# Kernel optimization log

Hardware: AMD Instinct MI355X
Metric: run time of the kernel (lower is better)

## Reference

```python
import jax, jax.numpy as jnp
import numpy as np
import math

B, L, D, H = 2, 2048, 1024, 16
DK = D // H

def setup_inputs() -> dict:
    key = jax.random.key(0)
    ks = jax.random.split(key, 12)
    s = 1.0 / math.sqrt(D)
    inp = {
        "Q": jax.random.normal(ks[0], (B, L, D), jnp.float32),
        "K": jax.random.normal(ks[1], (B, L, D), jnp.float32),
        "V": jax.random.normal(ks[2], (B, L, D), jnp.float32),
        "mask": jnp.tril(jnp.ones((L, L), jnp.bool_))[None, None],  # [1,1,L,L] causal
        "Wq_w": jax.random.normal(ks[3], (D, D), jnp.float32) * s,
        "Wq_b": jnp.zeros((D,), jnp.float32),
        "Wk_w": jax.random.normal(ks[4], (D, D), jnp.float32) * s,
        "Wk_b": jnp.zeros((D,), jnp.float32),
        "Wv_w": jax.random.normal(ks[5], (D, D), jnp.float32) * s,
        "Wv_b": jnp.zeros((D,), jnp.float32),
        "fc_w": jax.random.normal(ks[6], (D, D), jnp.float32) * s,
        "fc_b": jnp.zeros((D,), jnp.float32),
    }
    return inp

def reference(Q, K, V, mask, Wq_w, Wq_b, Wk_w, Wk_b, Wv_w, Wv_b, fc_w, fc_b):
    # torch Linear: y = x @ W.T + b
    def split_heads(x):
        return x.reshape(B, L, H, DK).transpose(0, 2, 1, 3)  # [B,H,L,DK]
    q = split_heads(Q @ Wq_w.T + Wq_b)
    k = split_heads(K @ Wk_w.T + Wk_b)
    v = split_heads(V @ Wv_w.T + Wv_b)
    scores = jnp.einsum("bhqd,bhkd->bhqk", q, k) / math.sqrt(DK)
    scores = jnp.where(mask, scores, jnp.float32(-1e9))
    attn = jax.nn.softmax(scores, axis=-1)
    out = jnp.einsum("bhqk,bhkd->bhqd", attn, v)
    out = out.transpose(0, 2, 1, 3).reshape(B, L, D)
    return out @ fc_w.T + fc_b
```

## Files before the change

kernel.cpp:

```cpp
#include <hip/hip_runtime.h>
#include <hip/hip_bf16.h>
#include <math.h>

typedef __attribute__((ext_vector_type(8))) short short8;
typedef __attribute__((ext_vector_type(4))) float float4v;

static constexpr int Bc = 2, Lc = 2048, Dc = 1024, Hc = 16;
static constexpr float C1 = 0.125f * 1.44269504088896f;
static constexpr float C2 = -8.0f * 1.44269504088896f;

__device__ __forceinline__ short f2bf(float x) {
    unsigned int b = __float_as_uint(x);
    return (short)((b + 0x7FFFu + ((b >> 16) & 1u)) >> 16);
}

__device__ __forceinline__ void gld16(const void* g, void* l) {
    __builtin_amdgcn_global_load_lds(
        (const __attribute__((address_space(1))) unsigned int*)g,
        (__attribute__((address_space(3))) unsigned int*)l, 16, 0, 0);
}

__global__ __launch_bounds__(256) void cvt_all(
    const float* q, const float* k, const float* v,
    const float* wq, const float* wk, const float* wv, const float* fw,
    short* qo, short* ko, short* vo,
    short* wqo, short* wko, short* wvo, short* fwo)
{
    const int z = blockIdx.y;
    const float* s; short* d; int n;
    switch (z) {
        case 0: s = q;  d = qo;  n = Bc*Lc*Dc; break;
        case 1: s = k;  d = ko;  n = Bc*Lc*Dc; break;
        case 2: s = v;  d = vo;  n = Bc*Lc*Dc; break;
        case 3: s = wq; d = wqo; n = Dc*Dc; break;
        case 4: s = wk; d = wko; n = Dc*Dc; break;
        case 5: s = wv; d = wvo; n = Dc*Dc; break;
        default: s = fw; d = fwo; n = Dc*Dc; break;
    }
    const int idx = (blockIdx.x * 256 + threadIdx.x) * 8;
    if (idx >= n) return;
    float4 lo = *reinterpret_cast<const float4*>(s + idx);
    float4 hi = *reinterpret_cast<const float4*>(s + idx + 4);
    short8 o = short8{f2bf(lo.x), f2bf(lo.y), f2bf(lo.z), f2bf(lo.w),
                      f2bf(hi.x), f2bf(hi.y), f2bf(hi.z), f2bf(hi.w)};
    *reinterpret_cast<short8*>(d + idx) = o;
}

struct GemmCtx {
    int lane, w, wm, wn, quad, l16, bm0, bn0, lrow, loct;
};
__device__ __forceinline__ void gemm_core(
    const short* __restrict__ A, const short* __restrict__ Bt,
    short* As, short* Bs, const GemmCtx& c, float4v acc[4][4])
{
    const int K = Dc;
    for (int k0 = 0; k0 < K; k0 += 32) {
#pragma unroll
        for (int rep = 0; rep < 2; ++rep) {
            const int rb = (c.w + 4 * rep) * 16;
            gld16(A  + (size_t)(c.bm0 + rb + c.lrow) * K + k0 + c.loct * 8, &As[rb * 32]);
            gld16(Bt + (size_t)(c.bn0 + rb + c.lrow) * K + k0 + c.loct * 8, &Bs[rb * 32]);
        }
        __syncthreads();
        short8 af[4], bf[4];
#pragma unroll
        for (int i = 0; i < 4; ++i)
            af[i] = *reinterpret_cast<const short8*>(&As[(c.wm * 64 + i * 16 + c.l16) * 32 + c.quad * 8]);
#pragma unroll
        for (int j = 0; j < 4; ++j)
            bf[j] = *reinterpret_cast<const short8*>(&Bs[(c.wn * 64 + j * 16 + c.l16) * 32 + c.quad * 8]);
#pragma unroll
        for (int i = 0; i < 4; ++i)
#pragma unroll
            for (int j = 0; j < 4; ++j)
                acc[i][j] = __builtin_amdgcn_mfma_f32_16x16x32_bf16(af[i], bf[j], acc[i][j], 0, 0, 0);
        __syncthreads();
    }
}
__device__ __forceinline__ GemmCtx make_ctx() {
    GemmCtx c;
    const int tid = threadIdx.x;
    c.lane = tid & 63; c.w = tid >> 6;
    c.wm = c.w >> 1;   c.wn = c.w & 1;
    c.quad = c.lane >> 4; c.l16 = c.lane & 15;
    c.bm0 = blockIdx.y * 128; c.bn0 = blockIdx.x * 128;
    c.lrow = c.lane >> 2; c.loct = c.lane & 3;
    return c;
}

__global__ __launch_bounds__(256, 2) void qkv_gemm(
    const short* __restrict__ Qb, const short* __restrict__ Kb, const short* __restrict__ Vb,
    const short* __restrict__ Wq, const short* __restrict__ Wk, const short* __restrict__ Wv,
    const float* __restrict__ bq, const float* __restrict__ bk, const float* __restrict__ bv,
    short* __restrict__ q_ws, short* __restrict__ k_ws, short* __restrict__ vT_ws)
{
    __shared__ short As[128 * 32];
    __shared__ short Bs[128 * 32];
    const int z = blockIdx.z;
    const short* A    = (z == 0) ? Qb : (z == 1) ? Kb : Vb;
    const short* Bt   = (z == 0) ? Wq : (z == 1) ? Wk : Wv;
    const float* bias = (z == 0) ? bq : (z == 1) ? bk : bv;

    GemmCtx c = make_ctx();
    float4v acc[4][4] = {};
    gemm_core(A, Bt, As, Bs, c, acc);

    if (z < 2) {
        short* C = (z == 0) ? q_ws : k_ws;
#pragma unroll
        for (int j = 0; j < 4; ++j) {
            const int col = c.bn0 + c.wn * 64 + j * 16 + c.l16;
            const float bv2 = bias[col];
#pragma unroll
            for (int i = 0; i < 4; ++i)
#pragma unroll
                for (int r = 0; r < 4; ++r) {
                    const int row = c.bm0 + c.wm * 64 + i * 16 + c.quad * 4 + r;
                    C[(size_t)row * Dc + col] = f2bf(acc[i][j][r] + bv2);
                }
        }
    } else {
#pragma unroll
        for (int j = 0; j < 4; ++j) {
            const int col = c.bn0 + c.wn * 64 + j * 16 + c.l16;
            const float bv2 = bias[col];
            const int hh = col >> 6, d = col & 63;
#pragma unroll
            for (int i = 0; i < 4; ++i)
#pragma unroll
                for (int r = 0; r < 4; ++r) {
                    const int row = c.bm0 + c.wm * 64 + i * 16 + c.quad * 4 + r;
                    const int b = row >> 11, l = row & 2047;
                    vT_ws[((size_t)((b * 16 + hh) * 64 + d)) * Lc + l] = f2bf(acc[i][j][r] + bv2);
                }
        }
    }
}

__global__ __launch_bounds__(256, 2) void out_gemm(
    const short* __restrict__ A, const short* __restrict__ Bt,
    const float* __restrict__ bias, float* __restrict__ C)
{
    __shared__ short As[128 * 32];
    __shared__ short Bs[128 * 32];
    GemmCtx c = make_ctx();
    float4v acc[4][4] = {};
    gemm_core(A, Bt, As, Bs, c, acc);
#pragma unroll
    for (int j = 0; j < 4; ++j) {
        const int col = c.bn0 + c.wn * 64 + j * 16 + c.l16;
        const float bv2 = bias[col];
#pragma unroll
        for (int i = 0; i < 4; ++i)
#pragma unroll
            for (int r = 0; r < 4; ++r) {
                const int row = c.bm0 + c.wm * 64 + i * 16 + c.quad * 4 + r;
                C[(size_t)row * Dc + col] = acc[i][j][r] + bv2;
            }
    }
}

__global__ __launch_bounds__(256, 2) void attn_flash3(
    const short* __restrict__ q_ws,
    const short* __restrict__ k_ws,
    const short* __restrict__ vT_ws,
    short* __restrict__ o_ws)
{
    __shared__ short Ks[64 * 64];
    __shared__ short Vs[80 * 64];
    __shared__ short Ps[4][16 * 40];

    const int tid  = threadIdx.x;
    const int lane = tid & 63;
    const int w    = tid >> 6;
    const int quad = lane >> 4;
    const int l16  = lane & 15;
    const int l7   = l16 & 7;

    const int id = blockIdx.x;
    const int p  = id & 15;
    const int bh = id >> 4;
    const int b  = bh >> 4, h = bh & 15;

    for (int i = tid; i < 16 * 64; i += 256) {
        const int row = 64 + (i >> 6);
        const int col = i & 63;
        const int oct = col >> 3;
        Vs[(row * 8 + (oct ^ (row & 7))) * 8 + (col & 7)] =
            (row == 64) ? (short)0x3F80 : (short)0;
    }

    const int srow = lane >> 3;
    const int soct = lane & 7;
    const size_t khead  = (size_t)(b * Lc) * Dc + h * 64;
    const size_t vthead = (size_t)(bh * 64) * Lc;
    const int xoct0 = quad ^ l7;
    const int xoct1 = (4 + quad) ^ l7;

#pragma unroll 1
    for (int ph = 0; ph < 2; ++ph) {
        const int qi  = ph ? (31 - p) : p;
        const int q0  = qi * 64;
        const int qw0 = q0 + w * 16;

        short8 qf[2];
        {
            const size_t base = ((size_t)(b * Lc + qw0 + l16)) * Dc + h * 64;
            qf[0] = *reinterpret_cast<const short8*>(&q_ws[base + quad * 8]);
            qf[1] = *reinterpret_cast<const short8*>(&q_ws[base + 32 + quad * 8]);
        }

        float4v o_acc[5] = {};

        for (int kb = 0; kb <= qi; ++kb) {
#pragma unroll
            for (int rep = 0; rep < 2; ++rep) {
                const int issue = w * 2 + rep;
                const int grow = issue * 8 + srow;
                const int goct = soct ^ (grow & 7);
                gld16(k_ws + khead + (size_t)(kb * 64 + grow) * Dc + goct * 8,
                      &Ks[issue * 512]);
                gld16(vT_ws + vthead + (size_t)grow * Lc + kb * 64 + goct * 8,
                      &Vs[issue * 512]);
            }
            __syncthreads();

            short8 vf[5][2];
#pragma unroll
            for (int dt = 0; dt < 5; ++dt) {
                vf[dt][0] = *reinterpret_cast<const short8*>(&Vs[(dt * 16 + l16) * 64 + xoct0 * 8]);
                vf[dt][1] = *reinterpret_cast<const short8*>(&Vs[(dt * 16 + l16) * 64 + xoct1 * 8]);
            }

#pragma unroll
            for (int pair = 0; pair < 2; ++pair) {
                if (kb * 64 + pair * 32 <= qw0 + 15) {
#pragma unroll
                    for (int tt = 0; tt < 2; ++tt) {
                        const int t = pair * 2 + tt;
                        short8 kf0 = *reinterpret_cast<const short8*>(&Ks[(t * 16 + l16) * 64 + xoct0 * 8]);
                        short8 kf1 = *reinterpret_cast<const short8*>(&Ks[(t * 16 + l16) * 64 + xoct1 * 8]);
                        float4v sv = {};
                        sv = __builtin_amdgcn_mfma_f32_16x16x32_bf16(qf[0], kf0, sv, 0, 0, 0);
                        sv = __builtin_amdgcn_mfma_f32_16x16x32_bf16(qf[1], kf1, sv, 0, 0, 0);
                        const int kcol = kb * 64 + t * 16 + l16;
#pragma unroll
                        for (int r = 0; r < 4; ++r) {
                            const int qrow = qw0 + quad * 4 + r;
                            const float pv = (kcol <= qrow) ? exp2f(fmaf(sv[r], C1, C2)) : 0.f;
                            Ps[w][(quad * 4 + r) * 40 + tt * 16 + l16] =
                                (short)(__float_as_uint(pv) >> 16);
                        }
                    }
                    asm volatile("s_waitcnt lgkmcnt(0)" ::: "memory");
                    short8 pf = *reinterpret_cast<const short8*>(&Ps[w][l16 * 40 + quad * 8]);
#pragma unroll
                    for (int dt = 0; dt < 5; ++dt)
                        o_acc[dt] = __builtin_amdgcn_mfma_f32_16x16x32_bf16(pf, vf[dt][pair], o_acc[dt], 0, 0, 0);
                }
            }
            __syncthreads();
        }

#pragma unroll
        for (int r = 0; r < 4; ++r) {
            const float lsum = __shfl(o_acc[4][r], quad << 4, 64);
            const float inv = 1.f / lsum;
            const int qrow = qw0 + quad * 4 + r;
#pragma unroll
            for (int dt = 0; dt < 4; ++dt)
                o_ws[((size_t)(b * Lc + qrow)) * Dc + h * 64 + dt * 16 + l16] =
                    f2bf(o_acc[dt][r] * inv);
        }
    }
}

extern "C" void kernel_launch(void* const* d_in, const int* in_sizes, int n_in,
                              void* d_out, int out_size, void* d_ws, size_t ws_size,
                              hipStream_t stream)
{
    const float* Q = (const float*)d_in[0];
    const float* K = (const float*)d_in[1];
    const float* V = (const float*)d_in[2];

    int w0 = -1;
    for (int i = 3; i + 8 <= n_in; ++i) {
        bool ok = true;
        for (int j = 0; j < 4 && ok; ++j)
            ok = (in_sizes[i + 2 * j] == Dc * Dc) && (in_sizes[i + 2 * j + 1] == Dc);
        if (ok) { w0 = i; break; }
    }
    if (w0 < 0) w0 = (n_in >= 12) ? 4 : 3;

    const float* Wq_w = (const float*)d_in[w0 + 0];
    const float* Wq_b = (const float*)d_in[w0 + 1];
    const float* Wk_w = (const float*)d_in[w0 + 2];
    const float* Wk_b = (const float*)d_in[w0 + 3];
    const float* Wv_w = (const float*)d_in[w0 + 4];
    const float* Wv_b = (const float*)d_in[w0 + 5];
    const float* fc_w = (const float*)d_in[w0 + 6];
    const float* fc_b = (const float*)d_in[w0 + 7];
    float* out = (float*)d_out;

    const size_t nel = (size_t)Bc * Lc * Dc;
    const size_t nw  = (size_t)Dc * Dc;
    short* p = (short*)d_ws;
    short* xq   = p;  p += nel;
    short* xk   = p;  p += nel;
    short* xv   = p;  p += nel;
    short* wqb  = p;  p += nw;
    short* wkb  = p;  p += nw;
    short* wvb  = p;  p += nw;
    short* fwb  = p;  p += nw;
    short* q_ws = p;  p += nel;
    short* k_ws = p;  p += nel;
    short* vT_ws= p;  p += nel;
    short* a_ws = xq;

    cvt_all<<<dim3(2048, 7), 256, 0, stream>>>(
        Q, K, V, Wq_w, Wk_w, Wv_w, fc_w, xq, xk, xv, wqb, wkb, wvb, fwb);

    qkv_gemm<<<dim3(8, 32, 3), 256, 0, stream>>>(
        xq, xk, xv, wqb, wkb, wvb, Wq_b, Wk_b, Wv_b, q_ws, k_ws, vT_ws);

    attn_flash3<<<dim3(512), 256, 0, stream>>>(q_ws, k_ws, vT_ws, a_ws);

    out_gemm<<<dim3(8, 32), 256, 0, stream>>>(a_ws, fwb, fc_b, out);
}
```

Before: 246.1 us.

## Double-buffer K/V tiles and keep P in registers via transposed score MFMA

```diff
diff --git a/kernel.cpp b/kernel.cpp
--- a/kernel.cpp
+++ b/kernel.cpp
@@ -3,7 +3,9 @@
 #include <math.h>
 
 typedef __attribute__((ext_vector_type(8))) short short8;
+typedef __attribute__((ext_vector_type(4))) short short4v;
 typedef __attribute__((ext_vector_type(4))) float float4v;
+typedef __attribute__((ext_vector_type(2))) unsigned int uint2v;
 
 static constexpr int Bc = 2, Lc = 2048, Dc = 1024, Hc = 16;
 static constexpr float C1 = 0.125f * 1.44269504088896f;
@@ -160,15 +162,14 @@
     }
 }
 
-__global__ __launch_bounds__(256, 2) void attn_flash3(
+__global__ __launch_bounds__(256, 2) void attn_flash4(
     const short* __restrict__ q_ws,
     const short* __restrict__ k_ws,
     const short* __restrict__ vT_ws,
     short* __restrict__ o_ws)
 {
-    __shared__ short Ks[64 * 64];
-    __shared__ short Vs[80 * 64];
-    __shared__ short Ps[4][16 * 40];
+    __shared__ short Ks[2][64 * 64];
+    __shared__ short Vs[2][64 * 64];
 
     const int tid  = threadIdx.x;
     const int lane = tid & 63;
@@ -182,14 +183,6 @@
     const int bh = id >> 4;
     const int b  = bh >> 4, h = bh & 15;
 
-    for (int i = tid; i < 16 * 64; i += 256) {
-        const int row = 64 + (i >> 6);
-        const int col = i & 63;
-        const int oct = col >> 3;
-        Vs[(row * 8 + (oct ^ (row & 7))) * 8 + (col & 7)] =
-            (row == 64) ? (short)0x3F80 : (short)0;
-    }
-
     const int srow = lane >> 3;
     const int soct = lane & 7;
     const size_t khead  = (size_t)(b * Lc) * Dc + h * 64;
@@ -197,11 +190,28 @@
     const int xoct0 = quad ^ l7;
     const int xoct1 = (4 + quad) ^ l7;
 
+    const short onev = (l16 == 0) ? (short)0x3F80 : (short)0;
+    const short4v vb4 = short4v{onev, onev, onev, onev};
+
+    auto stage = [&](int tile, int buf) {
+#pragma unroll
+        for (int rep = 0; rep < 2; ++rep) {
+            const int issue = w * 2 + rep;
+            const int grow = issue * 8 + srow;
+            const int goct = soct ^ (grow & 7);
+            gld16(k_ws + khead + (size_t)(tile * 64 + grow) * Dc + goct * 8,
+                  &Ks[buf][issue * 512]);
+            gld16(vT_ws + vthead + (size_t)grow * Lc + tile * 64 + goct * 8,
+                  &Vs[buf][issue * 512]);
+        }
+    };
+
 #pragma unroll 1
     for (int ph = 0; ph < 2; ++ph) {
         const int qi  = ph ? (31 - p) : p;
         const int q0  = qi * 64;
         const int qw0 = q0 + w * 16;
+        const int qrow = qw0 + l16;
 
         short8 qf[2];
         {
@@ -212,64 +222,68 @@
 
         float4v o_acc[5] = {};
 
+        stage(0, 0);
+
+#pragma unroll 1
         for (int kb = 0; kb <= qi; ++kb) {
-#pragma unroll
-            for (int rep = 0; rep < 2; ++rep) {
-                const int issue = w * 2 + rep;
-                const int grow = issue * 8 + srow;
-                const int goct = soct ^ (grow & 7);
-                gld16(k_ws + khead + (size_t)(kb * 64 + grow) * Dc + goct * 8,
-                      &Ks[issue * 512]);
-                gld16(vT_ws + vthead + (size_t)grow * Lc + kb * 64 + goct * 8,
-                      &Vs[issue * 512]);
+            const int cur = kb & 1;
+            if (kb < qi) {
+                stage(kb + 1, cur ^ 1);
+                asm volatile("s_waitcnt vmcnt(4)" ::: "memory");
+            } else {
+                asm volatile("s_waitcnt vmcnt(0)" ::: "memory");
             }
-            __syncthreads();
-
-            short8 vf[5][2];
-#pragma unroll
-            for (int dt = 0; dt < 5; ++dt) {
-                vf[dt][0] = *reinterpret_cast<const short8*>(&Vs[(dt * 16 + l16) * 64 + xoct0 * 8]);
-                vf[dt][1] = *reinterpret_cast<const short8*>(&Vs[(dt * 16 + l16) * 64 + xoct1 * 8]);
-            }
-
-#pragma unroll
-            for (int pair = 0; pair < 2; ++pair) {
-                if (kb * 64 + pair * 32 <= qw0 + 15) {
-#pragma unroll
-                    for (int tt = 0; tt < 2; ++tt) {
-                        const int t = pair * 2 + tt;
-                        short8 kf0 = *reinterpret_cast<const short8*>(&Ks[(t * 16 + l16) * 64 + xoct0 * 8]);
-                        short8 kf1 = *reinterpret_cast<const short8*>(&Ks[(t * 16 + l16) * 64 + xoct1 * 8]);
-                        float4v sv = {};
-                        sv = __builtin_amdgcn_mfma_f32_16x16x32_bf16(qf[0], kf0, sv, 0, 0, 0);
-                        sv = __builtin_amdgcn_mfma_f32_16x16x32_bf16(qf[1], kf1, sv, 0, 0, 0);
-                        const int kcol = kb * 64 + t * 16 + l16;
-#pragma unroll
-                        for (int r = 0; r < 4; ++r) {
-                            const int qrow = qw0 + quad * 4 + r;
-                            const float pv = (kcol <= qrow) ? exp2f(fmaf(sv[r], C1, C2)) : 0.f;
-                            Ps[w][(quad * 4 + r) * 40 + tt * 16 + l16] =
-                                (short)(__float_as_uint(pv) >> 16);
-                        }
+            __builtin_amdgcn_s_barrier();
+            asm volatile("" ::: "memory");
+
+            const short* Kc = &Ks[cur][0];
+            const short* Vc = &Vs[cur][0];
+
+#pragma unroll
+            for (int t = 0; t < 4; ++t) {
+                if (kb * 64 + t * 16 <= qw0 + 15) {
+                    short8 kf0 = *reinterpret_cast<const short8*>(&Kc[(t * 16 + l16) * 64 + xoct0 * 8]);
+                    short8 kf1 = *reinterpret_cast<const short8*>(&Kc[(t * 16 + l16) * 64 + xoct1 * 8]);
+                    float4v sv = {};
+                    sv = __builtin_amdgcn_mfma_f32_16x16x32_bf16(kf0, qf[0], sv, 0, 0, 0);
+                    sv = __builtin_amdgcn_mfma_f32_16x16x32_bf16(kf1, qf[1], sv, 0, 0, 0);
+
+                    short4v vb[4];
+#pragma unroll
+                    for (int dt = 0; dt < 4; ++dt)
+                        vb[dt] = *reinterpret_cast<const short4v*>(
+                            &Vc[(dt * 16 + l16) * 64 + ((2 * t + (quad >> 1)) ^ l7) * 8 + (quad & 1) * 4]);
+
+                    const int kbase = kb * 64 + t * 16 + quad * 4;
+                    unsigned u[4];
+#pragma unroll
+                    for (int r = 0; r < 4; ++r) {
+                        const float pv = (kbase + r <= qrow)
+                                       ? exp2f(fmaf(sv[r], C1, C2)) : 0.f;
+                        u[r] = __float_as_uint(pv);
                     }
-                    asm volatile("s_waitcnt lgkmcnt(0)" ::: "memory");
-                    short8 pf = *reinterpret_cast<const short8*>(&Ps[w][l16 * 40 + quad * 8]);
-#pragma unroll
-                    for (int dt = 0; dt < 5; ++dt)
-                        o_acc[dt] = __builtin_amdgcn_mfma_f32_16x16x32_bf16(pf, vf[dt][pair], o_acc[dt], 0, 0, 0);
+                    const uint2v pu = {(u[1] & 0xFFFF0000u) | (u[0] >> 16),
+                                       (u[3] & 0xFFFF0000u) | (u[2] >> 16)};
+                    const short4v pa = __builtin_bit_cast(short4v, pu);
+
+#pragma unroll
+                    for (int dt = 0; dt < 4; ++dt)
+                        o_acc[dt] = __builtin_amdgcn_mfma_f32_16x16x16bf16_1k(pa, vb[dt], o_acc[dt], 0, 0, 0);
+                    o_acc[4] = __builtin_amdgcn_mfma_f32_16x16x16bf16_1k(pa, vb4, o_acc[4], 0, 0, 0);
                 }
             }
-            __syncthreads();
+            asm volatile("" ::: "memory");
+            __builtin_amdgcn_s_barrier();
         }
 
 #pragma unroll
         for (int r = 0; r < 4; ++r) {
             const float lsum = __shfl(o_acc[4][r], quad << 4, 64);
             const float inv = 1.f / lsum;
-            const int qrow = qw0 + quad * 4 + r;
+            const int qr = qw0 + quad * 4 + r;
 #pragma unroll
             for (int dt = 0; dt < 4; ++dt)
-                o_ws[((size_t)(b * Lc + qrow)) * Dc + h * 64 + dt * 16 + l16] =
+                o_ws[((size_t)(b * Lc + qr)) * Dc + h * 64 + dt * 16 + l16] =
                     f2bf(o_acc[dt][r] * inv);
         }
     }
@@ -323,7 +337,7 @@
     qkv_gemm<<<dim3(8, 32, 3), 256, 0, stream>>>(
         xq, xk, xv, wqb, wkb, wvb, Wq_b, Wk_b, Wv_b, q_ws, k_ws, vT_ws);
 
-    attn_flash3<<<dim3(512), 256, 0, stream>>>(q_ws, k_ws, vT_ws, a_ws);
+    attn_flash4<<<dim3(512), 256, 0, stream>>>(q_ws, k_ws, vT_ws, a_ws);
 
     out_gemm<<<dim3(8, 32), 256, 0, stream>>>(a_ws, fwb, fc_b, out);
 }
```

New measurement: 247.7 us. No clear change (+0.7%).
